# Optimization experiments

Measured on AMD Instinct MI355X. Metric: run time of the kernel, lower is better.

The kernel has to match this reference:

```python
import jax, jax.numpy as jnp
import numpy as np

B, T, E = 16, 400, 768
P, H, A, L, M = 256, 1024, 128, 32, 80  # prenet, lstm, attn, loc-feat, mel dims
LSTM_IN = P + E  # 1024
PROJ_IN = H + E  # 1792 (decoder_state cat step_attention)


def setup_inputs() -> dict:
    key = jax.random.key(0)
    ks = jax.random.split(key, 32)
    s = 0.02
    rn = lambda k, shp: jax.random.normal(k, shp, jnp.float32) * s
    return {
        "x": jax.random.normal(ks[0], (B, T, E), jnp.float32),
        # PreNet
        "prenet_w1": rn(ks[1], (P, M)), "prenet_b1": jnp.zeros((P,), jnp.float32),
        "prenet_w2": rn(ks[2], (P, P)), "prenet_b2": jnp.zeros((P,), jnp.float32),
        # 2-layer LSTM (torch gate order i,f,g,o)
        "lstm_wih0": rn(ks[3], (4 * H, LSTM_IN)), "lstm_whh0": rn(ks[4], (4 * H, H)),
        "lstm_bih0": jnp.zeros((4 * H,), jnp.float32), "lstm_bhh0": jnp.zeros((4 * H,), jnp.float32),
        "lstm_wih1": rn(ks[5], (4 * H, H)), "lstm_whh1": rn(ks[6], (4 * H, H)),
        "lstm_bih1": jnp.zeros((4 * H,), jnp.float32), "lstm_bhh1": jnp.zeros((4 * H,), jnp.float32),
        # Location-sensitive attention
        "att_W_w": rn(ks[7], (A, H)), "att_W_b": jnp.zeros((A,), jnp.float32),
        "att_V_w": rn(ks[8], (A, E)),
        "att_U_w": rn(ks[9], (A, L)),
        "att_F_w": rn(ks[10], (L, 1, 31)),  # conv1d OIH, kernel 31, pad 15
        "att_v_w": rn(ks[11], (A,)),
        # projections
        "proj_w": rn(ks[12], (M, PROJ_IN)), "proj_b": jnp.zeros((M,), jnp.float32),
        "stop_w": rn(ks[13], (1, PROJ_IN)), "stop_b": jnp.zeros((1,), jnp.float32),
        # PostNet conv2d kernels (OIHW), kernel (1,5), pad (0,2)
        "pn_w1": rn(ks[14], (256, 1, 1, 5)), "pn_b1": jnp.zeros((256,), jnp.float32),
        "pn_w2": rn(ks[15], (256, 256, 1, 5)), "pn_b2": jnp.zeros((256,), jnp.float32),
        "pn_w3": rn(ks[16], (256, 256, 1, 5)), "pn_b3": jnp.zeros((256,), jnp.float32),
        "pn_w4": rn(ks[17], (1, 256, 1, 5)), "pn_b4": jnp.zeros((1,), jnp.float32),
    }


def _lstm_cell(xin, h, c, wih, whh, bih, bhh):
    z = xin @ wih.T + bih + h @ whh.T + bhh
    i, f, g, o = jnp.split(z, 4, axis=-1)
    c = jax.nn.sigmoid(f) * c + jax.nn.sigmoid(i) * jnp.tanh(g)
    h = jax.nn.sigmoid(o) * jnp.tanh(c)
    return h, c


def _conv2d(y, w, b):
    out = jax.lax.conv_general_dilated(y, w, (1, 1), [(0, 0), (2, 2)],
                                       dimension_numbers=("NCHW", "OIHW", "NCHW"))
    return out + b[None, :, None, None]


def reference(x, prenet_w1, prenet_b1, prenet_w2, prenet_b2,
              lstm_wih0, lstm_whh0, lstm_bih0, lstm_bhh0,
              lstm_wih1, lstm_whh1, lstm_bih1, lstm_bhh1,
              att_W_w, att_W_b, att_V_w, att_U_w, att_F_w, att_v_w,
              proj_w, proj_b, stop_w, stop_b,
              pn_w1, pn_b1, pn_w2, pn_b2, pn_w3, pn_b3, pn_w4, pn_b4):
    b, t, e = x.shape
    Vh = jnp.einsum("bte,ae->bta", x, att_V_w)  # precomputed once (self.Vh cache)

    def step(carry, _):
        step_in, step_att, h0, c0, h1, c1, cum = carry
        # PreNet (dropout = identity in eval)
        p = jax.nn.relu(step_in @ prenet_w1.T + prenet_b1)
        p = jax.nn.relu(p @ prenet_w2.T + prenet_b2)
        # 2-layer LSTM step on cat(prenet, prev attention context)
        lstm_in = jnp.concatenate([p, step_att], axis=-1)
        h0, c0 = _lstm_cell(lstm_in, h0, c0, lstm_wih0, lstm_whh0, lstm_bih0, lstm_bhh0)
        h1, c1 = _lstm_cell(h0, h1, c1, lstm_wih1, lstm_whh1, lstm_bih1, lstm_bhh1)
        dec = h1  # [B, H]
        lin_in = jnp.concatenate([dec, step_att], axis=-1)  # [B, H+E]
        out = lin_in @ proj_w.T + proj_b      # [B, M]
        stop = lin_in @ stop_w.T + stop_b     # [B, 1]
        # location-sensitive attention
        Ws = dec @ att_W_w.T + att_W_b        # [B, A]
        loc = jax.lax.conv_general_dilated(cum[:, None, :], att_F_w, (1,), [(15, 15)],
                                           dimension_numbers=("NCH", "OIH", "NCH"))  # [B, L, T]
        Uf = jnp.einsum("blt,al->bta", loc, att_U_w)  # [B, T, A]
        energies = jnp.tanh(Ws[:, None, :] + Vh + Uf) @ att_v_w  # [B, T]
        aw = jax.nn.softmax(energies, axis=1)
        ctx = jnp.einsum("bt,bte->be", aw, x)  # [B, E]
        cum = cum + aw
        return (out, ctx, h0, c0, h1, c1, cum), out

    z = lambda *shp: jnp.zeros(shp, x.dtype)
    carry0 = (z(b, M), z(b, E), z(b, H), z(b, H), z(b, H), z(b, H), z(b, t))
    _, outs = jax.lax.scan(step, carry0, None, length=t)  # [T, B, M]
    mel = jnp.transpose(outs, (1, 0, 2))[:, None, :, :]  # [B, 1, T, M]
    # PostNet with residual
    y = jnp.tanh(_conv2d(mel, pn_w1, pn_b1))
    y = jnp.tanh(_conv2d(y, pn_w2, pn_b2))
    y = jnp.tanh(_conv2d(y, pn_w3, pn_b3))
    y = _conv2d(y, pn_w4, pn_b4) + mel
    return y
```

## Files before the change

kernel.cpp:

```cpp
#include <hip/hip_runtime.h>
#include <stdint.h>
#include <stddef.h>

#define B 16
#define T 400
#define E 768
#define PDIM 256
#define H 1024
#define ADIM 128
#define LDIM 32
#define MDIM 80

typedef unsigned short u16;
typedef __attribute__((ext_vector_type(8))) short short8v;
typedef __attribute__((ext_vector_type(4))) float float4v;

__device__ __forceinline__ float bf2f(u16 u){
  union { uint32_t i; float f; } v; v.i = ((uint32_t)u) << 16; return v.f;
}
__device__ __forceinline__ u16 f2bf(float f){
  union { float f; uint32_t i; } v; v.f = f;
  uint32_t x = v.i;
  return (u16)((x + 0x7FFFu + ((x >> 16) & 1u)) >> 16);
}
__device__ __forceinline__ float fast_sig(float x){ return 1.f/(1.f+__expf(-x)); }
__device__ __forceinline__ float fast_tanh(float x){ float e=__expf(2.f*x); return 1.f - 2.f/(e+1.f); }

template<bool F32>
__device__ __forceinline__ float ld1(const void* p, size_t i){
  if constexpr(F32){ float v; __builtin_memcpy(&v, (const float*)p + i, 4); return v; }
  else { u16 h; __builtin_memcpy(&h, (const u16*)p + i, 2); return bf2f(h); }
}
template<bool F32>
__device__ __forceinline__ void ld4(const void* p, size_t i, float o[4]){
  if constexpr(F32){ __builtin_memcpy(o, (const float*)p + i, 16); }
  else {
    uint2 u; __builtin_memcpy(&u, (const u16*)p + i, 8);
    o[0]=bf2f((u16)(u.x & 0xffffu)); o[1]=bf2f((u16)(u.x >> 16));
    o[2]=bf2f((u16)(u.y & 0xffffu)); o[3]=bf2f((u16)(u.y >> 16));
  }
}
template<bool F32>
__device__ __forceinline__ void st1(void* p, size_t i, float v){
  if constexpr(F32) ((float*)p)[i] = v; else ((u16*)p)[i] = f2bf(v);
}

__global__ void k_detect(const uint32_t* __restrict__ x, int* flag){
  uint32_t w = x[threadIdx.x];
  float v = bf2f((u16)(w & 0xffffu));
  int bad = (fabsf(v) < 1e4f) ? 0 : 1;
  __shared__ int s[256];
  s[threadIdx.x] = bad;
  __syncthreads();
  for(int st=128; st>0; st>>=1){ if(threadIdx.x<st) s[threadIdx.x]+=s[threadIdx.x+st]; __syncthreads(); }
  if(threadIdx.x==0) *flag = (s[0] >= 8) ? 1 : 0;
}

__global__ void k_zero(float* p, int n){
  int i = blockIdx.x*256 + threadIdx.x;
  if(i < n) p[i] = 0.f;
}

template<bool F32>
__device__ __forceinline__ void init_prenet_body(const void* w2, const void* b1, const void* b2,
                                                 float* lstm_in){
  __shared__ float p1[PDIM];
  int j = threadIdx.x;
  p1[j] = fmaxf(ld1<F32>(b1, j), 0.f);
  __syncthreads();
  float acc = ld1<F32>(b2, j);
  for(int k=0;k<PDIM;k+=4){
    float w[4]; ld4<F32>(w2, (size_t)j*PDIM+k, w);
    acc += w[0]*p1[k]+w[1]*p1[k+1]+w[2]*p1[k+2]+w[3]*p1[k+3];
  }
  float p2 = fmaxf(acc, 0.f);
  for(int b=0;b<B;b++) lstm_in[b*H + j] = p2;
}
__global__ void k_init_prenet(const void* w2, const void* b1, const void* b2,
                              float* lstm_in, const int* dtf){
  if(*dtf) init_prenet_body<true>(w2,b1,b2,lstm_in);
  else     init_prenet_body<false>(w2,b1,b2,lstm_in);
}

template<bool F32>
__device__ __forceinline__ void vh_body(const void* __restrict__ x, const void* __restrict__ Vw,
                                        float* __restrict__ Vh){
  int bt = blockIdx.x;
  __shared__ float xr[E];
  for(int i=threadIdx.x;i<E;i+=128) xr[i] = ld1<F32>(x, (size_t)bt*E + i);
  __syncthreads();
  int a = threadIdx.x;
  float acc = 0.f;
#pragma unroll 4
  for(int k=0;k<E;k+=4){
    float w[4]; ld4<F32>(Vw, (size_t)a*E+k, w);
    acc += w[0]*xr[k]+w[1]*xr[k+1]+w[2]*xr[k+2]+w[3]*xr[k+3];
  }
  Vh[(size_t)bt*ADIM + a] = acc;
}
__global__ void k_vh(const void* __restrict__ x, const void* __restrict__ Vw,
                     float* __restrict__ Vh, const int* dtf){
  if(*dtf) vh_body<true>(x,Vw,Vh); else vh_body<false>(x,Vw,Vh);
}

template<bool F32>
__device__ __forceinline__ void lstm_body(
    const void* __restrict__ wih, const void* __restrict__ whh,
    const void* __restrict__ bih, const void* __restrict__ bhh,
    const float* __restrict__ in_x, const float* __restrict__ in_h,
    float* __restrict__ c_io, float* __restrict__ h_out,
    const float* __restrict__ cum, const void* __restrict__ Fw,
    const void* __restrict__ Uw, float* __restrict__ Uf)
{
  if(blockIdx.x < 1024){
    int j = blockIdx.x;
    int lane = threadIdx.x & 63;
    int wv = threadIdx.x >> 6;
    float acc[4][4];
#pragma unroll
    for(int g=0;g<4;g++)
#pragma unroll
      for(int bb=0;bb<4;bb++) acc[g][bb]=0.f;

#pragma unroll
    for(int it=0; it<4; it++){
      int k = it*256 + lane*4;
      float xi[4][4];
#pragma unroll
      for(int bb=0;bb<4;bb++) __builtin_memcpy(xi[bb], &in_x[(size_t)(wv*4+bb)*H + k], 16);
#pragma unroll
      for(int g=0;g<4;g++){
        float w[4]; ld4<F32>(wih, ((size_t)(g*H + j))*H + k, w);
#pragma unroll
        for(int bb=0;bb<4;bb++)
          acc[g][bb] += w[0]*xi[bb][0] + w[1]*xi[bb][1] + w[2]*xi[bb][2] + w[3]*xi[bb][3];
      }
    }
#pragma unroll
    for(int it=0; it<4; it++){
      int k = it*256 + lane*4;
      float xi[4][4];
#pragma unroll
      for(int bb=0;bb<4;bb++) __builtin_memcpy(xi[bb], &in_h[(size_t)(wv*4+bb)*H + k], 16);
#pragma unroll
      for(int g=0;g<4;g++){
        float w[4]; ld4<F32>(whh, ((size_t)(g*H + j))*H + k, w);
#pragma unroll
        for(int bb=0;bb<4;bb++)
          acc[g][bb] += w[0]*xi[bb][0] + w[1]*xi[bb][1] + w[2]*xi[bb][2] + w[3]*xi[bb][3];
      }
    }
#pragma unroll
    for(int off=1; off<64; off<<=1){
#pragma unroll
      for(int g=0;g<4;g++)
#pragma unroll
        for(int bb=0;bb<4;bb++)
          acc[g][bb] += __shfl_xor(acc[g][bb], off, 64);
    }
    if(lane == 0){
      float bsum[4];
#pragma unroll
      for(int g=0;g<4;g++) bsum[g] = ld1<F32>(bih, g*H+j) + ld1<F32>(bhh, g*H+j);
#pragma unroll
      for(int bb=0;bb<4;bb++){
        int b = wv*4+bb;
        float zi = acc[0][bb] + bsum[0];
        float zf = acc[1][bb] + bsum[1];
        float zg = acc[2][bb] + bsum[2];
        float zo = acc[3][bb] + bsum[3];
        float ig = fast_sig(zi), fg = fast_sig(zf);
        float gg = fast_tanh(zg), og = fast_sig(zo);
        float c = fg * c_io[(size_t)b*H+j] + ig*gg;
        c_io[(size_t)b*H+j] = c;
        h_out[(size_t)b*H+j] = og * fast_tanh(c);
      }
    }
  } else {
    int idx = blockIdx.x - 1024;
    int b = idx / 25, ch = idx % 25, t0 = ch*16;
    __shared__ float cumh[46];
    __shared__ float Fl[LDIM*31];
    __shared__ float Ul[ADIM*LDIM];
    __shared__ float loc[16*LDIM];
    int tid = threadIdx.x;
    if(tid < 46){ int g = t0 - 15 + tid; cumh[tid] = (g>=0 && g<T) ? cum[b*T+g] : 0.f; }
    for(int i=tid; i<LDIM*31; i+=256) Fl[i] = ld1<F32>(Fw, i);
    for(int i=tid; i<ADIM*LDIM; i+=256) Ul[i] = ld1<F32>(Uw, i);
    __syncthreads();
    for(int i=tid; i<16*LDIM; i+=256){
      int tl = i >> 5, l = i & 31;
      float s=0.f;
      for(int q=0;q<31;q++) s += cumh[tl+q]*Fl[l*31+q];
      loc[i] = s;
    }
    __syncthreads();
    int tl = tid >> 4, al = tid & 15;
    int t = t0 + tl;
#pragma unroll
    for(int aa=0; aa<8; aa++){
      int a = al*8 + aa;
      float s=0.f;
#pragma unroll
      for(int l=0;l<LDIM;l++) s += loc[tl*LDIM+l]*Ul[a*LDIM+l];
      Uf[((size_t)b*T + t)*ADIM + a] = s;
    }
  }
}
__global__ __launch_bounds__(256) void k_lstm(
    const void* wih, const void* whh, const void* bih, const void* bhh,
    const float* in_x, const float* in_h, float* c_io, float* h_out,
    const float* cum, const void* Fw, const void* Uw, float* Uf, const int* dtf)
{
  if(*dtf) lstm_body<true>(wih,whh,bih,bhh,in_x,in_h,c_io,h_out,cum,Fw,Uw,Uf);
  else     lstm_body<false>(wih,whh,bih,bhh,in_x,in_h,c_io,h_out,cum,Fw,Uw,Uf);
}

template<bool F32>
__device__ __forceinline__ void tail_body(int t,
    const float* __restrict__ h1, const float* __restrict__ att_r, float* __restrict__ att_w,
    float* __restrict__ lstm_in, float* __restrict__ cum,
    const float* __restrict__ Vh, const float* __restrict__ Uf,
    const void* __restrict__ x,
    const void* __restrict__ attW, const void* __restrict__ attWb, const void* __restrict__ attv,
    const void* __restrict__ projw, const void* __restrict__ projb,
    const void* __restrict__ pw1, const void* __restrict__ pb1,
    const void* __restrict__ pw2, const void* __restrict__ pb2,
    void* __restrict__ outp)
{
  int blk = blockIdx.x, tid = threadIdx.x;
  if(blk < 16){
    int b = blk;
    __shared__ float wsp[256];
    __shared__ float Ws[ADIM];
    __shared__ float vl[ADIM];
    __shared__ float el[T];
    __shared__ float red[256];
    {
      int a = tid >> 1, s = tid & 1;
      size_t base = (size_t)a*H + s*512;
      const float* hr = &h1[(size_t)b*H + s*512];
      float acc=0.f;
#pragma unroll 4
      for(int k=0;k<512;k+=4){
        float w[4]; ld4<F32>(attW, base+k, w);
        acc += w[0]*hr[k]+w[1]*hr[k+1]+w[2]*hr[k+2]+w[3]*hr[k+3];
      }
      wsp[tid]=acc;
    }
    __syncthreads();
    if(tid < ADIM){ Ws[tid] = wsp[2*tid]+wsp[2*tid+1] + ld1<F32>(attWb, tid); vl[tid] = ld1<F32>(attv, tid); }
    __syncthreads();
    for(int tt=tid; tt<T; tt+=256){
      const float* vh = &Vh[((size_t)b*T+tt)*ADIM];
      const float* uf = &Uf[((size_t)b*T+tt)*ADIM];
      float acc=0.f;
#pragma unroll 4
      for(int a=0;a<ADIM;a+=4){
        float v4[4], u4[4];
        __builtin_memcpy(v4, &vh[a], 16);
        __builtin_memcpy(u4, &uf[a], 16);
        acc += vl[a+0]*fast_tanh(Ws[a+0]+v4[0]+u4[0]);
        acc += vl[a+1]*fast_tanh(Ws[a+1]+v4[1]+u4[1]);
        acc += vl[a+2]*fast_tanh(Ws[a+2]+v4[2]+u4[2]);
        acc += vl[a+3]*fast_tanh(Ws[a+3]+v4[3]+u4[3]);
      }
      el[tt]=acc;
    }
    __syncthreads();
    float mx = -1e30f;
    for(int tt=tid; tt<T; tt+=256) mx = fmaxf(mx, el[tt]);
    red[tid]=mx; __syncthreads();
    for(int s=128;s>0;s>>=1){ if(tid<s) red[tid]=fmaxf(red[tid],red[tid+s]); __syncthreads(); }
    mx = red[0]; __syncthreads();
    float sum=0.f;
    for(int tt=tid; tt<T; tt+=256){ float ex=__expf(el[tt]-mx); el[tt]=ex; sum+=ex; }
    red[tid]=sum; __syncthreads();
    for(int s=128;s>0;s>>=1){ if(tid<s) red[tid]+=red[tid+s]; __syncthreads(); }
    float inv = 1.f/red[0];
    __syncthreads();
    for(int tt=tid; tt<T; tt+=256){ float aw = el[tt]*inv; el[tt]=aw; cum[b*T+tt] += aw; }
    __syncthreads();
    {
      float a0=0.f, a1=0.f, a2=0.f;
      const size_t xb = (size_t)b*T*E;
#pragma unroll 4
      for(int tt=0; tt<T; tt++){
        float aw = el[tt];
        size_t base = xb + (size_t)tt*E + tid;
        a0 += aw * ld1<F32>(x, base);
        a1 += aw * ld1<F32>(x, base+256);
        a2 += aw * ld1<F32>(x, base+512);
      }
      att_w[b*E + tid]       = a0;
      att_w[b*E + tid + 256] = a1;
      att_w[b*E + tid + 512] = a2;
      lstm_in[b*H + PDIM + tid]       = a0;
      lstm_in[b*H + PDIM + tid + 256] = a1;
      lstm_in[b*H + PDIM + tid + 512] = a2;
    }
  } else {
    int b = blk - 16;
    __shared__ float lin[H+E];
    __shared__ float pp[160];
    __shared__ float outl[MDIM];
    __shared__ float p1[PDIM];
    for(int i=tid;i<H;i+=256) lin[i] = h1[(size_t)b*H+i];
    for(int i=tid;i<E;i+=256) lin[H+i] = att_r[b*E+i];
    __syncthreads();
    if(tid < 160){
      int m = tid >> 1, s = tid & 1;
      size_t base = (size_t)m*1792 + s*896;
      const float* lr = &lin[s*896];
      float acc=0.f;
#pragma unroll 4
      for(int k=0;k<896;k+=4){
        float w[4]; ld4<F32>(projw, base+k, w);
        acc += w[0]*lr[k]+w[1]*lr[k+1]+w[2]*lr[k+2]+w[3]*lr[k+3];
      }
      pp[tid]=acc;
    }
    __syncthreads();
    if(tid < MDIM){
      float o = pp[2*tid]+pp[2*tid+1] + ld1<F32>(projb, tid);
      outl[tid]=o;
      st1<F32>(outp, ((size_t)b*T + t)*MDIM + tid, o);
    }
    __syncthreads();
    {
      float acc = ld1<F32>(pb1, tid);
#pragma unroll
      for(int k=0;k<MDIM;k+=4){
        float w[4]; ld4<F32>(pw1, (size_t)tid*MDIM+k, w);
        acc += w[0]*outl[k]+w[1]*outl[k+1]+w[2]*outl[k+2]+w[3]*outl[k+3];
      }
      p1[tid] = fmaxf(acc,0.f);
    }
    __syncthreads();
    {
      float acc = ld1<F32>(pb2, tid);
#pragma unroll 4
      for(int k=0;k<PDIM;k+=4){
        float w[4]; ld4<F32>(pw2, (size_t)tid*PDIM+k, w);
        acc += w[0]*p1[k]+w[1]*p1[k+1]+w[2]*p1[k+2]+w[3]*p1[k+3];
      }
      lstm_in[b*H + tid] = fmaxf(acc,0.f);
    }
  }
}
__global__ __launch_bounds__(256) void k_step_tail(int t,
    const float* h1, const float* att_r, float* att_w,
    float* lstm_in, float* cum, const float* Vh, const float* Uf,
    const void* x, const void* attW, const void* attWb, const void* attv,
    const void* projw, const void* projb,
    const void* pw1, const void* pb1, const void* pw2, const void* pb2,
    void* outp, const int* dtf)
{
  if(*dtf) tail_body<true>(t,h1,att_r,att_w,lstm_in,cum,Vh,Uf,x,attW,attWb,attv,projw,projb,pw1,pb1,pw2,pb2,outp);
  else     tail_body<false>(t,h1,att_r,att_w,lstm_in,cum,Vh,Uf,x,attW,attWb,attv,projw,projb,pw1,pb1,pw2,pb2,outp);
}

template<bool F32>
__device__ __forceinline__ void repack_body(const void* __restrict__ w, u16* __restrict__ wf){
  int blk = blockIdx.x;
  int ot = blk & 15, ic = (blk >> 4) & 7, kw = blk >> 7;
  int lane = threadIdx.x;
  int o = ot*16 + (lane & 15);
  int i0 = ic*32 + (lane >> 4)*8;
  size_t dst = ((size_t)blk*64 + lane)*8;
#pragma unroll
  for(int jj=0;jj<8;jj++)
    wf[dst+jj] = f2bf(ld1<F32>(w, ((size_t)o*256 + (i0+jj))*5 + kw));
}
__global__ void k_repack(const void* w, u16* wf, const int* dtf){
  if(*dtf) repack_body<true>(w,wf); else repack_body<false>(w,wf);
}

template<bool F32>
__device__ __forceinline__ void postnet_body(
    const void* __restrict__ w1, const void* __restrict__ b1,
    const u16* __restrict__ wf2, const void* __restrict__ b2,
    const u16* __restrict__ wf3, const void* __restrict__ b3,
    const void* __restrict__ w4, const void* __restrict__ b4,
    void* __restrict__ out)
{
  __shared__ u16 YT[88*264];
  __shared__ float mell[84];
  __shared__ float w4l[256*5];
  __shared__ float red4[160];
  int bt = blockIdx.x;
  int tid = threadIdx.x;
  if(tid < 84) mell[tid] = (tid>=2 && tid<82) ? ld1<F32>(out, (size_t)bt*MDIM + tid-2) : 0.f;
  for(int i=tid;i<256*5;i+=256) w4l[i] = ld1<F32>(w4, i);
  for(int i=tid;i<4*264;i+=256){
    int r = i/264, c = i - r*264;
    int row = (r<2)? r : 80+r;
    YT[row*264 + c] = 0;
  }
  __syncthreads();
  {
    float wr[5];
#pragma unroll
    for(int q=0;q<5;q++) wr[q] = ld1<F32>(w1, tid*5+q);
    float bb = ld1<F32>(b1, tid);
    for(int m=0;m<MDIM;m++){
      float s = bb;
#pragma unroll
      for(int q=0;q<5;q++) s += wr[q]*mell[m+q];
      YT[(m+2)*264 + tid] = f2bf(fast_tanh(s));
    }
  }
  __syncthreads();
  int lane = tid & 63, wv = tid >> 6;
  int lr = lane & 15, quad = lane >> 4;
  const u16* WF[2] = {wf2, wf3};
  const void* BS[2] = {b2, b3};
#pragma unroll 1
  for(int layer=0; layer<2; layer++){
    float4v acc[4][5];
#pragma unroll
    for(int ot=0;ot<4;ot++){
      int ob = (wv*4+ot)*16 + quad*4;
#pragma unroll
      for(int mt=0;mt<5;mt++)
#pragma unroll
        for(int r=0;r<4;r++) acc[ot][mt][r] = ld1<F32>(BS[layer], ob + r);
    }
    const u16* wf = WF[layer];
    for(int kw=0;kw<5;kw++){
      for(int ic=0;ic<8;ic++){
        short8v a[4];
#pragma unroll
        for(int ot=0;ot<4;ot++){
          size_t idx = ((size_t)(kw*128 + ic*16 + (wv*4+ot))*64 + lane)*8;
          __builtin_memcpy(&a[ot], &wf[idx], 16);
        }
        short8v bfr[5];
        int ib = ic*32 + quad*8;
#pragma unroll
        for(int mt=0;mt<5;mt++){
          int row = mt*16 + lr + kw;
          __builtin_memcpy(&bfr[mt], &YT[row*264 + ib], 16);
        }
#pragma unroll
        for(int ot=0;ot<4;ot++)
#pragma unroll
          for(int mt=0;mt<5;mt++)
            acc[ot][mt] = __builtin_amdgcn_mfma_f32_16x16x32_bf16(a[ot], bfr[mt], acc[ot][mt], 0,0,0);
      }
    }
    __syncthreads();
#pragma unroll
    for(int ot=0;ot<4;ot++){
      int ob = (wv*4+ot)*16 + quad*4;
#pragma unroll
      for(int mt=0;mt<5;mt++){
        int row = mt*16 + lr + 2;
        u16 pk[4];
#pragma unroll
        for(int r=0;r<4;r++) pk[r] = f2bf(fast_tanh(acc[ot][mt][r]));
        __builtin_memcpy(&YT[row*264 + ob], pk, 8);
      }
    }
    __syncthreads();
  }
  if(tid < 160){
    int m = tid >> 1, s = tid & 1;
    float accv = 0.f;
    for(int i = s*128; i < s*128+128; i++){
#pragma unroll
      for(int q=0;q<5;q++) accv += w4l[i*5+q] * bf2f(YT[(m+q)*264 + i]);
    }
    red4[tid] = accv;
  }
  __syncthreads();
  if(tid < MDIM){
    float o = red4[2*tid] + red4[2*tid+1] + ld1<F32>(b4, 0) + mell[tid+2];
    st1<F32>(out, (size_t)bt*MDIM + tid, o);
  }
}
__global__ __launch_bounds__(256) void k_postnet(
    const void* w1, const void* b1, const u16* wf2, const void* b2,
    const u16* wf3, const void* b3, const void* w4, const void* b4,
    void* out, const int* dtf)
{
  if(*dtf) postnet_body<true>(w1,b1,wf2,b2,wf3,b3,w4,b4,out);
  else     postnet_body<false>(w1,b1,wf2,b2,wf3,b3,w4,b4,out);
}

extern "C" void kernel_launch(void* const* d_in, const int* in_sizes, int n_in,
                              void* d_out, int out_size, void* d_ws, size_t ws_size,
                              hipStream_t stream)
{
  (void)in_sizes; (void)n_in; (void)out_size; (void)ws_size;
  const void* x    = d_in[0];
  const void* pw1  = d_in[1];
  const void* pb1  = d_in[2];
  const void* pw2  = d_in[3];
  const void* pb2  = d_in[4];
  const void* wih0 = d_in[5];
  const void* whh0 = d_in[6];
  const void* bih0 = d_in[7];
  const void* bhh0 = d_in[8];
  const void* wih1 = d_in[9];
  const void* whh1 = d_in[10];
  const void* bih1 = d_in[11];
  const void* bhh1 = d_in[12];
  const void* attW = d_in[13];
  const void* attWb= d_in[14];
  const void* attV = d_in[15];
  const void* attU = d_in[16];
  const void* attF = d_in[17];
  const void* attv = d_in[18];
  const void* projw= d_in[19];
  const void* projb= d_in[20];
  const void* pnw1 = d_in[23];
  const void* pnb1 = d_in[24];
  const void* pnw2 = d_in[25];
  const void* pnb2 = d_in[26];
  const void* pnw3 = d_in[27];
  const void* pnb3 = d_in[28];
  const void* pnw4 = d_in[29];
  const void* pnb4 = d_in[30];

  float* base = (float*)d_ws;
  size_t off = 4;
  int* dtf = (int*)d_ws;
  float* Vh   = base + off; off += (size_t)B*T*ADIM;
  float* Uf   = base + off; off += (size_t)B*T*ADIM;
  float* h0a  = base + off; off += B*H;
  float* h0b  = base + off; off += B*H;
  float* h1a  = base + off; off += B*H;
  float* h1b  = base + off; off += B*H;
  float* c0   = base + off; off += B*H;
  float* c1   = base + off; off += B*H;
  float* att0 = base + off; off += B*E;
  float* att1 = base + off; off += B*E;
  float* lstm_in = base + off; off += B*H;
  float* cum  = base + off; off += B*T;
  u16* wf2 = (u16*)(base + off); off += (5*8*16*64*8)/2;
  u16* wf3 = (u16*)(base + off); off += (5*8*16*64*8)/2;

  k_detect<<<1, 256, 0, stream>>>((const uint32_t*)x, dtf);
  int nzero = 6*B*H + 2*B*E + B*H + B*T;
  k_zero<<<(nzero+255)/256, 256, 0, stream>>>(h0a, nzero);
  k_init_prenet<<<1, 256, 0, stream>>>(pw2, pb1, pb2, lstm_in, dtf);
  k_vh<<<B*T, 128, 0, stream>>>(x, attV, Vh, dtf);
  k_repack<<<640, 64, 0, stream>>>(pnw2, wf2, dtf);
  k_repack<<<640, 64, 0, stream>>>(pnw3, wf3, dtf);

  for(int t=0; t<T; t++){
    float* h0r = (t&1)? h0b : h0a;
    float* h0w = (t&1)? h0a : h0b;
    float* h1r = (t&1)? h1b : h1a;
    float* h1w = (t&1)? h1a : h1b;
    float* attr = (t&1)? att1 : att0;
    float* attw = (t&1)? att0 : att1;
    k_lstm<<<1424, 256, 0, stream>>>(wih0, whh0, bih0, bhh0, lstm_in, h0r, c0, h0w,
                                     cum, attF, attU, Uf, dtf);
    k_lstm<<<1024, 256, 0, stream>>>(wih1, whh1, bih1, bhh1, h0w, h1r, c1, h1w,
                                     cum, attF, attU, Uf, dtf);
    k_step_tail<<<32, 256, 0, stream>>>(t, h1w, attr, attw, lstm_in, cum, Vh, Uf, x,
                                        attW, attWb, attv, projw, projb,
                                        pw1, pb1, pw2, pb2, d_out, dtf);
  }
  k_postnet<<<B*T, 256, 0, stream>>>(pnw1, pnb1, wf2, pnb2, wf3, pnb3,
                                     pnw4, pnb4, d_out, dtf);
}
```

Measured before the change: 59.38 ms.

## Replace per-step kernel launches with a persistent kernel using hierarchical grid barriers

The 1200 per-timestep launches (two LSTM layers plus a tail) become a single persistent kernel of 512 blocks that loops over timesteps and separates phases with a two-level atomic grid barrier. The tail is split so context computation and Uf recompute run as a separate, wider parallel phase, with attention weights staged in global memory. This removes launch overhead and per-launch idle gaps, but adds four grid barriers per step and assumes all 512 blocks are co-resident. Uf is now zero-initialised because the location update runs after attention instead of inside the layer-0 LSTM launch.

```diff
diff --git a/kernel.cpp b/kernel.cpp
--- a/kernel.cpp
+++ b/kernel.cpp
@@ -11,6 +11,8 @@
 #define LDIM 32
 #define MDIM 80
 
+#define NBP 512
+
 typedef unsigned short u16;
 typedef __attribute__((ext_vector_type(8))) short short8v;
 typedef __attribute__((ext_vector_type(4))) float float4v;
@@ -101,263 +103,6 @@
 __global__ void k_vh(const void* __restrict__ x, const void* __restrict__ Vw,
                      float* __restrict__ Vh, const int* dtf){
   if(*dtf) vh_body<true>(x,Vw,Vh); else vh_body<false>(x,Vw,Vh);
-}
-
-template<bool F32>
-__device__ __forceinline__ void lstm_body(
-    const void* __restrict__ wih, const void* __restrict__ whh,
-    const void* __restrict__ bih, const void* __restrict__ bhh,
-    const float* __restrict__ in_x, const float* __restrict__ in_h,
-    float* __restrict__ c_io, float* __restrict__ h_out,
-    const float* __restrict__ cum, const void* __restrict__ Fw,
-    const void* __restrict__ Uw, float* __restrict__ Uf)
-{
-  if(blockIdx.x < 1024){
-    int j = blockIdx.x;
-    int lane = threadIdx.x & 63;
-    int wv = threadIdx.x >> 6;
-    float acc[4][4];
-#pragma unroll
-    for(int g=0;g<4;g++)
-#pragma unroll
-      for(int bb=0;bb<4;bb++) acc[g][bb]=0.f;
-
-#pragma unroll
-    for(int it=0; it<4; it++){
-      int k = it*256 + lane*4;
-      float xi[4][4];
-#pragma unroll
-      for(int bb=0;bb<4;bb++) __builtin_memcpy(xi[bb], &in_x[(size_t)(wv*4+bb)*H + k], 16);
-#pragma unroll
-      for(int g=0;g<4;g++){
-        float w[4]; ld4<F32>(wih, ((size_t)(g*H + j))*H + k, w);
-#pragma unroll
-        for(int bb=0;bb<4;bb++)
-          acc[g][bb] += w[0]*xi[bb][0] + w[1]*xi[bb][1] + w[2]*xi[bb][2] + w[3]*xi[bb][3];
-      }
-    }
-#pragma unroll
-    for(int it=0; it<4; it++){
-      int k = it*256 + lane*4;
-      float xi[4][4];
-#pragma unroll
-      for(int bb=0;bb<4;bb++) __builtin_memcpy(xi[bb], &in_h[(size_t)(wv*4+bb)*H + k], 16);
-#pragma unroll
-      for(int g=0;g<4;g++){
-        float w[4]; ld4<F32>(whh, ((size_t)(g*H + j))*H + k, w);
-#pragma unroll
-        for(int bb=0;bb<4;bb++)
-          acc[g][bb] += w[0]*xi[bb][0] + w[1]*xi[bb][1] + w[2]*xi[bb][2] + w[3]*xi[bb][3];
-      }
-    }
-#pragma unroll
-    for(int off=1; off<64; off<<=1){
-#pragma unroll
-      for(int g=0;g<4;g++)
-#pragma unroll
-        for(int bb=0;bb<4;bb++)
-          acc[g][bb] += __shfl_xor(acc[g][bb], off, 64);
-    }
-    if(lane == 0){
-      float bsum[4];
-#pragma unroll
-      for(int g=0;g<4;g++) bsum[g] = ld1<F32>(bih, g*H+j) + ld1<F32>(bhh, g*H+j);
-#pragma unroll
-      for(int bb=0;bb<4;bb++){
-        int b = wv*4+bb;
-        float zi = acc[0][bb] + bsum[0];
-        float zf = acc[1][bb] + bsum[1];
-        float zg = acc[2][bb] + bsum[2];
-        float zo = acc[3][bb] + bsum[3];
-        float ig = fast_sig(zi), fg = fast_sig(zf);
-        float gg = fast_tanh(zg), og = fast_sig(zo);
-        float c = fg * c_io[(size_t)b*H+j] + ig*gg;
-        c_io[(size_t)b*H+j] = c;
-        h_out[(size_t)b*H+j] = og * fast_tanh(c);
-      }
-    }
-  } else {
-    int idx = blockIdx.x - 1024;
-    int b = idx / 25, ch = idx % 25, t0 = ch*16;
-    __shared__ float cumh[46];
-    __shared__ float Fl[LDIM*31];
-    __shared__ float Ul[ADIM*LDIM];
-    __shared__ float loc[16*LDIM];
-    int tid = threadIdx.x;
-    if(tid < 46){ int g = t0 - 15 + tid; cumh[tid] = (g>=0 && g<T) ? cum[b*T+g] : 0.f; }
-    for(int i=tid; i<LDIM*31; i+=256) Fl[i] = ld1<F32>(Fw, i);
-    for(int i=tid; i<ADIM*LDIM; i+=256) Ul[i] = ld1<F32>(Uw, i);
-    __syncthreads();
-    for(int i=tid; i<16*LDIM; i+=256){
-      int tl = i >> 5, l = i & 31;
-      float s=0.f;
-      for(int q=0;q<31;q++) s += cumh[tl+q]*Fl[l*31+q];
-      loc[i] = s;
-    }
-    __syncthreads();
-    int tl = tid >> 4, al = tid & 15;
-    int t = t0 + tl;
-#pragma unroll
-    for(int aa=0; aa<8; aa++){
-      int a = al*8 + aa;
-      float s=0.f;
-#pragma unroll
-      for(int l=0;l<LDIM;l++) s += loc[tl*LDIM+l]*Ul[a*LDIM+l];
-      Uf[((size_t)b*T + t)*ADIM + a] = s;
-    }
-  }
-}
-__global__ __launch_bounds__(256) void k_lstm(
-    const void* wih, const void* whh, const void* bih, const void* bhh,
-    const float* in_x, const float* in_h, float* c_io, float* h_out,
-    const float* cum, const void* Fw, const void* Uw, float* Uf, const int* dtf)
-{
-  if(*dtf) lstm_body<true>(wih,whh,bih,bhh,in_x,in_h,c_io,h_out,cum,Fw,Uw,Uf);
-  else     lstm_body<false>(wih,whh,bih,bhh,in_x,in_h,c_io,h_out,cum,Fw,Uw,Uf);
-}
-
-template<bool F32>
-__device__ __forceinline__ void tail_body(int t,
-    const float* __restrict__ h1, const float* __restrict__ att_r, float* __restrict__ att_w,
-    float* __restrict__ lstm_in, float* __restrict__ cum,
-    const float* __restrict__ Vh, const float* __restrict__ Uf,
-    const void* __restrict__ x,
-    const void* __restrict__ attW, const void* __restrict__ attWb, const void* __restrict__ attv,
-    const void* __restrict__ projw, const void* __restrict__ projb,
-    const void* __restrict__ pw1, const void* __restrict__ pb1,
-    const void* __restrict__ pw2, const void* __restrict__ pb2,
-    void* __restrict__ outp)
-{
-  int blk = blockIdx.x, tid = threadIdx.x;
-  if(blk < 16){
-    int b = blk;
-    __shared__ float wsp[256];
-    __shared__ float Ws[ADIM];
-    __shared__ float vl[ADIM];
-    __shared__ float el[T];
-    __shared__ float red[256];
-    {
-      int a = tid >> 1, s = tid & 1;
-      size_t base = (size_t)a*H + s*512;
-      const float* hr = &h1[(size_t)b*H + s*512];
-      float acc=0.f;
-#pragma unroll 4
-      for(int k=0;k<512;k+=4){
-        float w[4]; ld4<F32>(attW, base+k, w);
-        acc += w[0]*hr[k]+w[1]*hr[k+1]+w[2]*hr[k+2]+w[3]*hr[k+3];
-      }
-      wsp[tid]=acc;
-    }
-    __syncthreads();
-    if(tid < ADIM){ Ws[tid] = wsp[2*tid]+wsp[2*tid+1] + ld1<F32>(attWb, tid); vl[tid] = ld1<F32>(attv, tid); }
-    __syncthreads();
-    for(int tt=tid; tt<T; tt+=256){
-      const float* vh = &Vh[((size_t)b*T+tt)*ADIM];
-      const float* uf = &Uf[((size_t)b*T+tt)*ADIM];
-      float acc=0.f;
-#pragma unroll 4
-      for(int a=0;a<ADIM;a+=4){
-        float v4[4], u4[4];
-        __builtin_memcpy(v4, &vh[a], 16);
-        __builtin_memcpy(u4, &uf[a], 16);
-        acc += vl[a+0]*fast_tanh(Ws[a+0]+v4[0]+u4[0]);
-        acc += vl[a+1]*fast_tanh(Ws[a+1]+v4[1]+u4[1]);
-        acc += vl[a+2]*fast_tanh(Ws[a+2]+v4[2]+u4[2]);
-        acc += vl[a+3]*fast_tanh(Ws[a+3]+v4[3]+u4[3]);
-      }
-      el[tt]=acc;
-    }
-    __syncthreads();
-    float mx = -1e30f;
-    for(int tt=tid; tt<T; tt+=256) mx = fmaxf(mx, el[tt]);
-    red[tid]=mx; __syncthreads();
-    for(int s=128;s>0;s>>=1){ if(tid<s) red[tid]=fmaxf(red[tid],red[tid+s]); __syncthreads(); }
-    mx = red[0]; __syncthreads();
-    float sum=0.f;
-    for(int tt=tid; tt<T; tt+=256){ float ex=__expf(el[tt]-mx); el[tt]=ex; sum+=ex; }
-    red[tid]=sum; __syncthreads();
-    for(int s=128;s>0;s>>=1){ if(tid<s) red[tid]+=red[tid+s]; __syncthreads(); }
-    float inv = 1.f/red[0];
-    __syncthreads();
-    for(int tt=tid; tt<T; tt+=256){ float aw = el[tt]*inv; el[tt]=aw; cum[b*T+tt] += aw; }
-    __syncthreads();
-    {
-      float a0=0.f, a1=0.f, a2=0.f;
-      const size_t xb = (size_t)b*T*E;
-#pragma unroll 4
-      for(int tt=0; tt<T; tt++){
-        float aw = el[tt];
-        size_t base = xb + (size_t)tt*E + tid;
-        a0 += aw * ld1<F32>(x, base);
-        a1 += aw * ld1<F32>(x, base+256);
-        a2 += aw * ld1<F32>(x, base+512);
-      }
-      att_w[b*E + tid]       = a0;
-      att_w[b*E + tid + 256] = a1;
-      att_w[b*E + tid + 512] = a2;
-      lstm_in[b*H + PDIM + tid]       = a0;
-      lstm_in[b*H + PDIM + tid + 256] = a1;
-      lstm_in[b*H + PDIM + tid + 512] = a2;
-    }
-  } else {
-    int b = blk - 16;
-    __shared__ float lin[H+E];
-    __shared__ float pp[160];
-    __shared__ float outl[MDIM];
-    __shared__ float p1[PDIM];
-    for(int i=tid;i<H;i+=256) lin[i] = h1[(size_t)b*H+i];
-    for(int i=tid;i<E;i+=256) lin[H+i] = att_r[b*E+i];
-    __syncthreads();
-    if(tid < 160){
-      int m = tid >> 1, s = tid & 1;
-      size_t base = (size_t)m*1792 + s*896;
-      const float* lr = &lin[s*896];
-      float acc=0.f;
-#pragma unroll 4
-      for(int k=0;k<896;k+=4){
-        float w[4]; ld4<F32>(projw, base+k, w);
-        acc += w[0]*lr[k]+w[1]*lr[k+1]+w[2]*lr[k+2]+w[3]*lr[k+3];
-      }
-      pp[tid]=acc;
-    }
-    __syncthreads();
-    if(tid < MDIM){
-      float o = pp[2*tid]+pp[2*tid+1] + ld1<F32>(projb, tid);
-      outl[tid]=o;
-      st1<F32>(outp, ((size_t)b*T + t)*MDIM + tid, o);
-    }
-    __syncthreads();
-    {
-      float acc = ld1<F32>(pb1, tid);
-#pragma unroll
-      for(int k=0;k<MDIM;k+=4){
-        float w[4]; ld4<F32>(pw1, (size_t)tid*MDIM+k, w);
-        acc += w[0]*outl[k]+w[1]*outl[k+1]+w[2]*outl[k+2]+w[3]*outl[k+3];
-      }
-      p1[tid] = fmaxf(acc,0.f);
-    }
-    __syncthreads();
-    {
-      float acc = ld1<F32>(pb2, tid);
-#pragma unroll 4
-      for(int k=0;k<PDIM;k+=4){
-        float w[4]; ld4<F32>(pw2, (size_t)tid*PDIM+k, w);
-        acc += w[0]*p1[k]+w[1]*p1[k+1]+w[2]*p1[k+2]+w[3]*p1[k+3];
-      }
-      lstm_in[b*H + tid] = fmaxf(acc,0.f);
-    }
-  }
-}
-__global__ __launch_bounds__(256) void k_step_tail(int t,
-    const float* h1, const float* att_r, float* att_w,
-    float* lstm_in, float* cum, const float* Vh, const float* Uf,
-    const void* x, const void* attW, const void* attWb, const void* attv,
-    const void* projw, const void* projb,
-    const void* pw1, const void* pb1, const void* pw2, const void* pb2,
-    void* outp, const int* dtf)
-{
-  if(*dtf) tail_body<true>(t,h1,att_r,att_w,lstm_in,cum,Vh,Uf,x,attW,attWb,attv,projw,projb,pw1,pb1,pw2,pb2,outp);
-  else     tail_body<false>(t,h1,att_r,att_w,lstm_in,cum,Vh,Uf,x,attW,attWb,attv,projw,projb,pw1,pb1,pw2,pb2,outp);
 }
 
 template<bool F32>
@@ -486,6 +231,314 @@
 {
   if(*dtf) postnet_body<true>(w1,b1,wf2,b2,wf3,b3,w4,b4,out);
   else     postnet_body<false>(w1,b1,wf2,b2,wf3,b3,w4,b4,out);
+}
+
+
+struct AttS { float wsp[256]; float Ws[ADIM]; float vl[ADIM]; float el[T]; float red[256]; };
+struct ProjS { float lin[H+E]; float pp[160]; float outl[MDIM]; float p1[PDIM]; };
+struct UfS  { float cumh[46]; float Fl[LDIM*31]; float Ul[ADIM*LDIM]; float loc[16*LDIM]; };
+struct CtxS { float aw[T]; };
+union SmemU { AttS att; ProjS proj; UfS uf; CtxS ctx; };
+
+template<bool F32>
+__device__ __forceinline__ void lstm_unit(int j,
+    const void* __restrict__ wih, const void* __restrict__ whh,
+    const void* __restrict__ bih, const void* __restrict__ bhh,
+    const float* __restrict__ in_x, const float* __restrict__ in_h,
+    float* __restrict__ c_io, float* __restrict__ h_out)
+{
+  int lane = threadIdx.x & 63;
+  int wv = threadIdx.x >> 6;
+  float acc[4][4];
+#pragma unroll
+  for(int g=0;g<4;g++)
+#pragma unroll
+    for(int bb=0;bb<4;bb++) acc[g][bb]=0.f;
+#pragma unroll
+  for(int it=0; it<4; it++){
+    int k = it*256 + lane*4;
+    float xi[4][4];
+#pragma unroll
+    for(int bb=0;bb<4;bb++) __builtin_memcpy(xi[bb], &in_x[(size_t)(wv*4+bb)*H + k], 16);
+#pragma unroll
+    for(int g=0;g<4;g++){
+      float w[4]; ld4<F32>(wih, ((size_t)(g*H + j))*H + k, w);
+#pragma unroll
+      for(int bb=0;bb<4;bb++)
+        acc[g][bb] += w[0]*xi[bb][0] + w[1]*xi[bb][1] + w[2]*xi[bb][2] + w[3]*xi[bb][3];
+    }
+  }
+#pragma unroll
+  for(int it=0; it<4; it++){
+    int k = it*256 + lane*4;
+    float xi[4][4];
+#pragma unroll
+    for(int bb=0;bb<4;bb++) __builtin_memcpy(xi[bb], &in_h[(size_t)(wv*4+bb)*H + k], 16);
+#pragma unroll
+    for(int g=0;g<4;g++){
+      float w[4]; ld4<F32>(whh, ((size_t)(g*H + j))*H + k, w);
+#pragma unroll
+      for(int bb=0;bb<4;bb++)
+        acc[g][bb] += w[0]*xi[bb][0] + w[1]*xi[bb][1] + w[2]*xi[bb][2] + w[3]*xi[bb][3];
+    }
+  }
+#pragma unroll
+  for(int off=1; off<64; off<<=1){
+#pragma unroll
+    for(int g=0;g<4;g++)
+#pragma unroll
+      for(int bb=0;bb<4;bb++)
+        acc[g][bb] += __shfl_xor(acc[g][bb], off, 64);
+  }
+  if(lane == 0){
+    float bsum[4];
+#pragma unroll
+    for(int g=0;g<4;g++) bsum[g] = ld1<F32>(bih, g*H+j) + ld1<F32>(bhh, g*H+j);
+#pragma unroll
+    for(int bb=0;bb<4;bb++){
+      int b = wv*4+bb;
+      float zi = acc[0][bb] + bsum[0];
+      float zf = acc[1][bb] + bsum[1];
+      float zg = acc[2][bb] + bsum[2];
+      float zo = acc[3][bb] + bsum[3];
+      float ig = fast_sig(zi), fg = fast_sig(zf);
+      float gg = fast_tanh(zg), og = fast_sig(zo);
+      float c = fg * c_io[(size_t)b*H+j] + ig*gg;
+      c_io[(size_t)b*H+j] = c;
+      h_out[(size_t)b*H+j] = og * fast_tanh(c);
+    }
+  }
+}
+
+template<bool F32>
+__device__ __forceinline__ void attn_unit(int b,
+    const float* __restrict__ h1,
+    const float* __restrict__ Vh, const float* __restrict__ Uf,
+    float* __restrict__ awg, float* __restrict__ cum,
+    const void* __restrict__ attW, const void* __restrict__ attWb,
+    const void* __restrict__ attv, AttS& S)
+{
+  int tid = threadIdx.x;
+  {
+    int a = tid >> 1, s = tid & 1;
+    size_t base = (size_t)a*H + s*512;
+    const float* hr = &h1[(size_t)b*H + s*512];
+    float acc=0.f;
+#pragma unroll 4
+    for(int k=0;k<512;k+=4){
+      float w[4]; ld4<F32>(attW, base+k, w);
+      acc += w[0]*hr[k]+w[1]*hr[k+1]+w[2]*hr[k+2]+w[3]*hr[k+3];
+    }
+    S.wsp[tid]=acc;
+  }
+  __syncthreads();
+  if(tid < ADIM){ S.Ws[tid] = S.wsp[2*tid]+S.wsp[2*tid+1] + ld1<F32>(attWb, tid); S.vl[tid] = ld1<F32>(attv, tid); }
+  __syncthreads();
+  for(int tt=tid; tt<T; tt+=256){
+    const float* vh = &Vh[((size_t)b*T+tt)*ADIM];
+    const float* uf = &Uf[((size_t)b*T+tt)*ADIM];
+    float acc=0.f;
+#pragma unroll 4
+    for(int a=0;a<ADIM;a+=4){
+      float v4[4], u4[4];
+      __builtin_memcpy(v4, &vh[a], 16);
+      __builtin_memcpy(u4, &uf[a], 16);
+      acc += S.vl[a+0]*fast_tanh(S.Ws[a+0]+v4[0]+u4[0]);
+      acc += S.vl[a+1]*fast_tanh(S.Ws[a+1]+v4[1]+u4[1]);
+      acc += S.vl[a+2]*fast_tanh(S.Ws[a+2]+v4[2]+u4[2]);
+      acc += S.vl[a+3]*fast_tanh(S.Ws[a+3]+v4[3]+u4[3]);
+    }
+    S.el[tt]=acc;
+  }
+  __syncthreads();
+  float mx = -1e30f;
+  for(int tt=tid; tt<T; tt+=256) mx = fmaxf(mx, S.el[tt]);
+  S.red[tid]=mx; __syncthreads();
+  for(int s=128;s>0;s>>=1){ if(tid<s) S.red[tid]=fmaxf(S.red[tid],S.red[tid+s]); __syncthreads(); }
+  mx = S.red[0]; __syncthreads();
+  float sum=0.f;
+  for(int tt=tid; tt<T; tt+=256){ float ex=__expf(S.el[tt]-mx); S.el[tt]=ex; sum+=ex; }
+  S.red[tid]=sum; __syncthreads();
+  for(int s=128;s>0;s>>=1){ if(tid<s) S.red[tid]+=S.red[tid+s]; __syncthreads(); }
+  float inv = 1.f/S.red[0];
+  __syncthreads();
+  for(int tt=tid; tt<T; tt+=256){ float a = S.el[tt]*inv; awg[b*T+tt]=a; cum[b*T+tt] += a; }
+}
+
+template<bool F32>
+__device__ __forceinline__ void proj_unit(int b, int t,
+    const float* __restrict__ h1, const float* __restrict__ att_r,
+    const void* __restrict__ projw, const void* __restrict__ projb,
+    const void* __restrict__ pw1, const void* __restrict__ pb1,
+    const void* __restrict__ pw2, const void* __restrict__ pb2,
+    float* __restrict__ lstm_in, void* __restrict__ outp, ProjS& S)
+{
+  int tid = threadIdx.x;
+  for(int i=tid;i<H;i+=256) S.lin[i] = h1[(size_t)b*H+i];
+  for(int i=tid;i<E;i+=256) S.lin[H+i] = att_r[b*E+i];
+  __syncthreads();
+  if(tid < 160){
+    int m = tid >> 1, s = tid & 1;
+    size_t base = (size_t)m*1792 + s*896;
+    const float* lr = &S.lin[s*896];
+    float acc=0.f;
+#pragma unroll 4
+    for(int k=0;k<896;k+=4){
+      float w[4]; ld4<F32>(projw, base+k, w);
+      acc += w[0]*lr[k]+w[1]*lr[k+1]+w[2]*lr[k+2]+w[3]*lr[k+3];
+    }
+    S.pp[tid]=acc;
+  }
+  __syncthreads();
+  if(tid < MDIM){
+    float o = S.pp[2*tid]+S.pp[2*tid+1] + ld1<F32>(projb, tid);
+    S.outl[tid]=o;
+    st1<F32>(outp, ((size_t)b*T + t)*MDIM + tid, o);
+  }
+  __syncthreads();
+  {
+    float acc = ld1<F32>(pb1, tid);
+#pragma unroll
+    for(int k=0;k<MDIM;k+=4){
+      float w[4]; ld4<F32>(pw1, (size_t)tid*MDIM+k, w);
+      acc += w[0]*S.outl[k]+w[1]*S.outl[k+1]+w[2]*S.outl[k+2]+w[3]*S.outl[k+3];
+    }
+    S.p1[tid] = fmaxf(acc,0.f);
+  }
+  __syncthreads();
+  {
+    float acc = ld1<F32>(pb2, tid);
+#pragma unroll 4
+    for(int k=0;k<PDIM;k+=4){
+      float w[4]; ld4<F32>(pw2, (size_t)tid*PDIM+k, w);
+      acc += w[0]*S.p1[k]+w[1]*S.p1[k+1]+w[2]*S.p1[k+2]+w[3]*S.p1[k+3];
+    }
+    lstm_in[b*H + tid] = fmaxf(acc,0.f);
+  }
+}
+
+template<bool F32>
+__device__ __forceinline__ void ctx_unit(int u,
+    const float* __restrict__ awg, const void* __restrict__ x,
+    float* __restrict__ att_w, float* __restrict__ lstm_in, float* __restrict__ awl)
+{
+  int b = u/3, cc = u%3;
+  int tid = threadIdx.x;
+  for(int i=tid;i<T;i+=256) awl[i] = awg[b*T+i];
+  __syncthreads();
+  int col = cc*256 + tid;
+  float a0 = 0.f;
+  const size_t xb = (size_t)b*T*E + col;
+#pragma unroll 4
+  for(int tt=0; tt<T; tt++) a0 += awl[tt] * ld1<F32>(x, xb + (size_t)tt*E);
+  att_w[b*E + col] = a0;
+  lstm_in[b*H + PDIM + col] = a0;
+}
+
+template<bool F32>
+__device__ __forceinline__ void uf_unit(int idx,
+    const float* __restrict__ cum, const void* __restrict__ Fw,
+    const void* __restrict__ Uw, float* __restrict__ Uf, UfS& S)
+{
+  int b = idx / 25, ch = idx % 25, t0 = ch*16;
+  int tid = threadIdx.x;
+  if(tid < 46){ int g = t0 - 15 + tid; S.cumh[tid] = (g>=0 && g<T) ? cum[b*T+g] : 0.f; }
+  for(int i=tid; i<LDIM*31; i+=256) S.Fl[i] = ld1<F32>(Fw, i);
+  for(int i=tid; i<ADIM*LDIM; i+=256) S.Ul[i] = ld1<F32>(Uw, i);
+  __syncthreads();
+  for(int i=tid; i<16*LDIM; i+=256){
+    int tl = i >> 5, l = i & 31;
+    float s=0.f;
+    for(int q=0;q<31;q++) s += S.cumh[tl+q]*S.Fl[l*31+q];
+    S.loc[i] = s;
+  }
+  __syncthreads();
+  int tl = tid >> 4, al = tid & 15;
+  int t = t0 + tl;
+#pragma unroll
+  for(int aa=0; aa<8; aa++){
+    int a = al*8 + aa;
+    float s=0.f;
+#pragma unroll
+    for(int l=0;l<LDIM;l++) s += S.loc[tl*LDIM+l]*S.Ul[a*LDIM+l];
+    Uf[((size_t)b*T + t)*ADIM + a] = s;
+  }
+}
+
+__device__ __forceinline__ void gbar(unsigned* leaf, unsigned* root, unsigned* gen){
+  __threadfence();
+  __syncthreads();
+  if(threadIdx.x == 0){
+    unsigned g = __hip_atomic_load(gen, __ATOMIC_RELAXED, __HIP_MEMORY_SCOPE_AGENT);
+    unsigned l = blockIdx.x & 31u;
+    unsigned target = gridDim.x >> 5;
+    unsigned r = __hip_atomic_fetch_add(&leaf[l*32u], 1u, __ATOMIC_RELAXED, __HIP_MEMORY_SCOPE_AGENT);
+    if(r == target - 1u){
+      __hip_atomic_store(&leaf[l*32u], 0u, __ATOMIC_RELAXED, __HIP_MEMORY_SCOPE_AGENT);
+      unsigned rr = __hip_atomic_fetch_add(root, 1u, __ATOMIC_RELAXED, __HIP_MEMORY_SCOPE_AGENT);
+      if(rr == 31u){
+        __hip_atomic_store(root, 0u, __ATOMIC_RELAXED, __HIP_MEMORY_SCOPE_AGENT);
+        __hip_atomic_fetch_add(gen, 1u, __ATOMIC_RELEASE, __HIP_MEMORY_SCOPE_AGENT);
+      }
+    }
+    long guard = 0;
+    while(__hip_atomic_load(gen, __ATOMIC_RELAXED, __HIP_MEMORY_SCOPE_AGENT) == g){
+      __builtin_amdgcn_s_sleep(4);
+      if(++guard > (1L<<24)) break;
+    }
+  }
+  __syncthreads();
+  __threadfence();
+}
+
+struct PP {
+  const void *wih0,*whh0,*bih0,*bhh0;
+  const void *wih1,*whh1,*bih1,*bhh1;
+  const void *attW,*attWb,*attv,*attF,*attU;
+  const void *projw,*projb,*pw1,*pb1,*pw2,*pb2;
+  const void *x;
+  float *Vh,*Uf,*h0a,*h0b,*h1a,*h1b,*c0,*c1,*att0,*att1,*lstm_in,*cum,*aw;
+  unsigned *barLeaf,*barRoot,*barGen;
+  void *outp;
+  const int* dtf;
+};
+
+template<bool F32>
+__device__ void persist_body(const PP& p){
+  __shared__ SmemU sm;
+  const int nb = gridDim.x;
+  float *h0r=p.h0a, *h0w=p.h0b, *h1r=p.h1a, *h1w=p.h1b, *attr=p.att0, *attw=p.att1;
+  for(int t=0; t<T; t++){
+    for(int j=blockIdx.x; j<H; j+=nb)
+      lstm_unit<F32>(j, p.wih0,p.whh0,p.bih0,p.bhh0, p.lstm_in, h0r, p.c0, h0w);
+    gbar(p.barLeaf, p.barRoot, p.barGen);
+    for(int j=blockIdx.x; j<H; j+=nb)
+      lstm_unit<F32>(j, p.wih1,p.whh1,p.bih1,p.bhh1, h0w, h1r, p.c1, h1w);
+    gbar(p.barLeaf, p.barRoot, p.barGen);
+    for(int u=blockIdx.x; u<32; u+=nb){
+      if(u < 16) attn_unit<F32>(u, h1w, p.Vh, p.Uf, p.aw, p.cum, p.attW, p.attWb, p.attv, sm.att);
+      else       proj_unit<F32>(u-16, t, h1w, attr, p.projw,p.projb,p.pw1,p.pb1,p.pw2,p.pb2,
+                                p.lstm_in, p.outp, sm.proj);
+      __syncthreads();
+    }
+    gbar(p.barLeaf, p.barRoot, p.barGen);
+    if(t+1 < T){
+      for(int u=blockIdx.x; u<448; u+=nb){
+        if(u < 48) ctx_unit<F32>(u, p.aw, p.x, attw, p.lstm_in, sm.ctx.aw);
+        else       uf_unit<F32>(u-48, p.cum, p.attF, p.attU, p.Uf, sm.uf);
+        __syncthreads();
+      }
+      gbar(p.barLeaf, p.barRoot, p.barGen);
+    }
+    float* tp;
+    tp=h0r; h0r=h0w; h0w=tp;
+    tp=h1r; h1r=h1w; h1w=tp;
+    tp=attr; attr=attw; attw=tp;
+  }
+}
+
+__global__ __launch_bounds__(256, 2) void k_persist(PP p){
+  if(*p.dtf) persist_body<true>(p); else persist_body<false>(p);
 }
 
 extern "C" void kernel_launch(void* const* d_in, const int* in_sizes, int n_in,
@@ -524,8 +577,8 @@
   const void* pnb4 = d_in[30];
 
   float* base = (float*)d_ws;
+  int* dtf = (int*)d_ws;
   size_t off = 4;
-  int* dtf = (int*)d_ws;
   float* Vh   = base + off; off += (size_t)B*T*ADIM;
   float* Uf   = base + off; off += (size_t)B*T*ADIM;
   float* h0a  = base + off; off += B*H;
@@ -538,32 +591,32 @@
   float* att1 = base + off; off += B*E;
   float* lstm_in = base + off; off += B*H;
   float* cum  = base + off; off += B*T;
+  float* aw   = base + off; off += B*T;
+  unsigned* bar = (unsigned*)(base + off); off += 1088;
   u16* wf2 = (u16*)(base + off); off += (5*8*16*64*8)/2;
   u16* wf3 = (u16*)(base + off); off += (5*8*16*64*8)/2;
 
   k_detect<<<1, 256, 0, stream>>>((const uint32_t*)x, dtf);
-  int nzero = 6*B*H + 2*B*E + B*H + B*T;
-  k_zero<<<(nzero+255)/256, 256, 0, stream>>>(h0a, nzero);
+  int nzero = (B*T*ADIM) + 6*B*H + 2*B*E + B*H + B*T + B*T + 1088;
+  k_zero<<<(nzero+255)/256, 256, 0, stream>>>(Uf, nzero);
   k_init_prenet<<<1, 256, 0, stream>>>(pw2, pb1, pb2, lstm_in, dtf);
   k_vh<<<B*T, 128, 0, stream>>>(x, attV, Vh, dtf);
   k_repack<<<640, 64, 0, stream>>>(pnw2, wf2, dtf);
   k_repack<<<640, 64, 0, stream>>>(pnw3, wf3, dtf);
 
-  for(int t=0; t<T; t++){
-    float* h0r = (t&1)? h0b : h0a;
-    float* h0w = (t&1)? h0a : h0b;
-    float* h1r = (t&1)? h1b : h1a;
-    float* h1w = (t&1)? h1a : h1b;
-    float* attr = (t&1)? att1 : att0;
-    float* attw = (t&1)? att0 : att1;
-    k_lstm<<<1424, 256, 0, stream>>>(wih0, whh0, bih0, bhh0, lstm_in, h0r, c0, h0w,
-                                     cum, attF, attU, Uf, dtf);
-    k_lstm<<<1024, 256, 0, stream>>>(wih1, whh1, bih1, bhh1, h0w, h1r, c1, h1w,
-                                     cum, attF, attU, Uf, dtf);
-    k_step_tail<<<32, 256, 0, stream>>>(t, h1w, attr, attw, lstm_in, cum, Vh, Uf, x,
-                                        attW, attWb, attv, projw, projb,
-                                        pw1, pb1, pw2, pb2, d_out, dtf);
-  }
+  PP p;
+  p.wih0=wih0; p.whh0=whh0; p.bih0=bih0; p.bhh0=bhh0;
+  p.wih1=wih1; p.whh1=whh1; p.bih1=bih1; p.bhh1=bhh1;
+  p.attW=attW; p.attWb=attWb; p.attv=attv; p.attF=attF; p.attU=attU;
+  p.projw=projw; p.projb=projb; p.pw1=pw1; p.pb1=pb1; p.pw2=pw2; p.pb2=pb2;
+  p.x=x;
+  p.Vh=Vh; p.Uf=Uf; p.h0a=h0a; p.h0b=h0b; p.h1a=h1a; p.h1b=h1b;
+  p.c0=c0; p.c1=c1; p.att0=att0; p.att1=att1; p.lstm_in=lstm_in; p.cum=cum; p.aw=aw;
+  p.barLeaf=bar; p.barRoot=bar+1024; p.barGen=bar+1056;
+  p.outp=d_out; p.dtf=dtf;
+
+  k_persist<<<NBP, 256, 0, stream>>>(p);
+
   k_postnet<<<B*T, 256, 0, stream>>>(pnw1, pnb1, wf2, pnb2, wf3, pnb3,
                                      pnw4, pnb4, d_out, dtf);
 }
```

After: 195.0 ms. +228.5%, slower.
